# Kernel optimization log

Measured on AMD Instinct MI355X. Metric: run time of the kernel, lower is better.

Reference implementation:

```python
import jax, jax.numpy as jnp
import numpy as np

N = 100_000   # nodes
E = 1_600_000 # edges (avg degree 16)
D = 64        # node feature / conv width
L = 3         # num conv layers
M = 128       # final mlp hidden
BN_EPS = 1e-5


def setup_inputs() -> dict:
    key = jax.random.key(0)
    ks = jax.random.split(key, 12)
    s = np.float32(1.0 / np.sqrt(D))
    sm = np.float32(1.0 / np.sqrt(M))
    return dict(
        x=jax.random.normal(ks[0], (N, D), jnp.float32),
        edge_src=jax.random.randint(ks[1], (E,), 0, N, dtype=jnp.int32),
        edge_dst=jax.random.randint(ks[2], (E,), 0, N, dtype=jnp.int32),
        W1=jax.random.normal(ks[3], (L, D, D), jnp.float32) * s,
        b1=jnp.zeros((L, D), jnp.float32),
        g1=jnp.ones((L, D), jnp.float32),
        be1=jnp.zeros((L, D), jnp.float32),
        W2=jax.random.normal(ks[4], (L, D, D), jnp.float32) * s,
        b2=jnp.zeros((L, D), jnp.float32),
        eps_gin=jnp.zeros((L,), jnp.float32),  # train_eps=True, init 0
        g_bn=jnp.ones((L, D), jnp.float32),
        b_bn=jnp.zeros((L, D), jnp.float32),
        Wf1=jax.random.normal(ks[5], (D, M), jnp.float32) * s,
        bf1=jnp.zeros((M,), jnp.float32),
        gf=jnp.ones((M,), jnp.float32),
        bef=jnp.zeros((M,), jnp.float32),
        Wf2=jax.random.normal(ks[6], (M, 1), jnp.float32) * sm,
        bf2=jnp.zeros((1,), jnp.float32),
    )


def _bn(h, g, b):
    # BatchNorm1d training-mode forward over node dim (biased variance)
    m = h.mean(axis=0)
    v = h.var(axis=0)
    return (h - m) * jax.lax.rsqrt(v + BN_EPS) * g + b


def reference(x, edge_src, edge_dst, W1, b1, g1, be1, W2, b2, eps_gin,
              g_bn, b_bn, Wf1, bf1, gf, bef, Wf2, bf2):
    for i in range(L):
        # GIN aggregation: sum of neighbor features (scatter-add over edges)
        agg = jax.ops.segment_sum(x[edge_src], edge_dst, num_segments=N)
        h = (1.0 + eps_gin[i]) * x + agg
        # GIN nn: Linear -> BatchNorm -> LeakyReLU -> Linear
        h = h @ W1[i] + b1[i]
        h = jax.nn.leaky_relu(_bn(h, g1[i], be1[i]))  # slope 0.01 = torch default
        x = h @ W2[i] + b2[i]
        # outer BatchNorm + activation on all but last conv layer
        if i != L - 1:
            x = jax.nn.leaky_relu(_bn(x, g_bn[i], b_bn[i]))
    # final head: Linear -> BN -> LeakyReLU -> Linear(->1), flatten
    h = x @ Wf1 + bf1
    h = jax.nn.leaky_relu(_bn(h, gf, bef))
    out = h @ Wf2 + bf2
    return out.ravel()  # [N]
```

## Files before the change

### kernel.cpp

```cpp
#include <hip/hip_runtime.h>

#define LRELU(x) ((x) > 0.0f ? (x) : 0.01f * (x))
#define UAF __uint_as_float
#define NSLOT 16

#if defined(__has_builtin)
#if __has_builtin(__builtin_amdgcn_fdot2_f32_bf16)
#define HAS_DOT2BF 1
#endif
#endif
#ifndef HAS_DOT2BF
#define HAS_DOT2BF 0
#endif

__device__ inline uint pack_bf16_rne(float x, float y) {
    uint lo = __float_as_uint(x);
    uint hi = __float_as_uint(y);
    lo = (lo + 0x7fffu + ((lo >> 16) & 1u)) >> 16;
    hi = (hi + 0x7fffu + ((hi >> 16) & 1u)) & 0xffff0000u;
    return lo | hi;
}

__device__ inline float dot2bf(uint a, uint b, float c) {
#if HAS_DOT2BF
    typedef __bf16 bf16x2 __attribute__((ext_vector_type(2)));
    return __builtin_amdgcn_fdot2_f32_bf16(__builtin_bit_cast(bf16x2, a),
                                           __builtin_bit_cast(bf16x2, b), c, false);
#else
    c += UAF(a << 16) * UAF(b << 16);
    c += UAF(a & 0xffff0000u) * UAF(b & 0xffff0000u);
    return c;
#endif
}

__global__ void zero_kernel(float* p, int n) {
    int i = blockIdx.x * blockDim.x + threadIdx.x;
    if (i < n) p[i] = 0.0f;
}

__global__ __launch_bounds__(256) void bhist_kernel(const int* __restrict__ dst,
                                                    int* __restrict__ bcnt, int E, int NB) {
    __shared__ int h[512];
    for (int i = threadIdx.x; i < NB; i += 256) h[i] = 0;
    __syncthreads();
    int base = blockIdx.x * 8192;
    int end = min(E, base + 8192);
    for (int e = base + threadIdx.x; e < end; e += 256) atomicAdd(&h[dst[e] >> 8], 1);
    __syncthreads();
    for (int i = threadIdx.x; i < NB; i += 256)
        if (h[i]) atomicAdd(&bcnt[i], h[i]);
}

__global__ __launch_bounds__(512) void bscan_kernel(const int* __restrict__ bcnt,
                                                    int* __restrict__ boff,
                                                    int* __restrict__ bcur, int NB) {
    __shared__ int sh[512];
    int t = threadIdx.x;
    int v = (t < NB) ? bcnt[t] : 0;
    sh[t] = v;
    __syncthreads();
    for (int o = 1; o < 512; o <<= 1) {
        int u = (t >= o) ? sh[t - o] : 0;
        __syncthreads();
        sh[t] += u;
        __syncthreads();
    }
    if (t < NB) {
        boff[t] = sh[t] - v;
        bcur[t] = sh[t] - v;
    }
}

__global__ __launch_bounds__(256) void bscatter_kernel(const int* __restrict__ src,
                                                       const int* __restrict__ dst,
                                                       int* __restrict__ bcur,
                                                       uint* __restrict__ pairs, int E, int NB) {
    __shared__ int h[512];
    __shared__ int bbase[512];
    for (int i = threadIdx.x; i < NB; i += 256) h[i] = 0;
    __syncthreads();
    int base = blockIdx.x * 8192;
    int end = min(E, base + 8192);
    for (int e = base + threadIdx.x; e < end; e += 256) atomicAdd(&h[dst[e] >> 8], 1);
    __syncthreads();
    for (int i = threadIdx.x; i < NB; i += 256) {
        bbase[i] = h[i] ? atomicAdd(&bcur[i], h[i]) : 0;
        h[i] = 0;
    }
    __syncthreads();
    for (int e = base + threadIdx.x; e < end; e += 256) {
        int d = dst[e];
        int b = d >> 8;
        int o = atomicAdd(&h[b], 1);
        pairs[bbase[b] + o] = ((uint)src[e] << 8) | (uint)(d & 255);
    }
}

__global__ __launch_bounds__(256) void bcsr_kernel(const uint* __restrict__ pairs,
                                                   const int* __restrict__ boff,
                                                   int* __restrict__ ptr, int* __restrict__ cnt,
                                                   int* __restrict__ nbr, int N, int NB, int E) {
    __shared__ int h[256];
    __shared__ int sc[256];
    int b = blockIdx.x;
    int lo = boff[b];
    int hi = (b + 1 < NB) ? boff[b + 1] : E;
    int t = threadIdx.x;
    h[t] = 0;
    __syncthreads();
    for (int i = lo + t; i < hi; i += 256) atomicAdd(&h[pairs[i] & 255u], 1);
    __syncthreads();
    int v = h[t];
    sc[t] = v;
    __syncthreads();
    for (int o = 1; o < 256; o <<= 1) {
        int u = (t >= o) ? sc[t - o] : 0;
        __syncthreads();
        sc[t] += u;
        __syncthreads();
    }
    int excl = sc[t] - v;
    int node = (b << 8) + t;
    if (node < N) {
        ptr[node] = lo + excl;
        cnt[node] = v;
    }
    __syncthreads();
    h[t] = excl;
    __syncthreads();
    for (int i = lo + t; i < hi; i += 256) {
        uint p = pairs[i];
        int ld = p & 255u;
        int o = atomicAdd(&h[ld], 1);
        nbr[lo + o] = (int)(p >> 8);
    }
}

__global__ __launch_bounds__(256) void to_bf16_kernel(const float* __restrict__ in,
                                                      uint* __restrict__ table, int n8) {
    int i = blockIdx.x * blockDim.x + threadIdx.x;
    if (i >= n8) return;
    float4 a = *(const float4*)&in[(size_t)i * 8];
    float4 b = *(const float4*)&in[(size_t)i * 8 + 4];
    uint4 p = make_uint4(pack_bf16_rne(a.x, a.y), pack_bf16_rne(a.z, a.w),
                         pack_bf16_rne(b.x, b.y), pack_bf16_rne(b.z, b.w));
    *(uint4*)&table[(size_t)i * 4] = p;
}

__global__ void finalize_kernel(const float* __restrict__ sums, const float* __restrict__ g,
                                const float* __restrict__ be, float* __restrict__ scale,
                                float* __restrict__ shift, int C, float invN) {
    int d = threadIdx.x;
    if (d >= C) return;
    float s = 0.0f, s2 = 0.0f;
    for (int k = 0; k < NSLOT; k++) {
        s += sums[k * 2 * C + d];
        s2 += sums[k * 2 * C + C + d];
    }
    float mean = s * invN;
    float var = s2 * invN - mean * mean;
    float sc = g[d] * rsqrtf(var + 1e-5f);
    scale[d] = sc;
    shift[d] = be[d] - mean * sc;
}

template <bool ACT>
__global__ __launch_bounds__(256) void gather_kernel(
    const uint* __restrict__ tb, const int* __restrict__ ptr, const int* __restrict__ cnt,
    const int* __restrict__ nbr, const float* __restrict__ eps_gin, int layer,
    const float* __restrict__ scale, const float* __restrict__ shift, uint* __restrict__ agg,
    int N) {
    int gtid = blockIdx.x * blockDim.x + threadIdx.x;
    int node = gtid >> 6;
    if (node >= N) return;
    int lane = threadIdx.x & 63;
    int half = lane >> 5;
    int sl = lane & 31;
    float sc0 = 1.0f, sh0 = 0.0f, sc1 = 1.0f, sh1 = 0.0f;
    if (ACT) {
        sc0 = scale[2 * sl + 0];
        sh0 = shift[2 * sl + 0];
        sc1 = scale[2 * sl + 1];
        sh1 = shift[2 * sl + 1];
    }
    int start = ptr[node];
    int deg = cnt[node];
    float a0 = 0.0f, a1 = 0.0f;
    int j = half;
    for (; j + 14 < deg; j += 16) {
        int ni[8];
        uint vv[8];
#pragma unroll
        for (int q = 0; q < 8; q++) ni[q] = nbr[start + j + 2 * q];
#pragma unroll
        for (int q = 0; q < 8; q++) vv[q] = tb[(size_t)ni[q] * 32 + sl];
#pragma unroll
        for (int q = 0; q < 8; q++) {
            float f0 = UAF(vv[q] << 16), f1 = UAF(vv[q] & 0xffff0000u);
            if (ACT) {
                f0 = LRELU(f0 * sc0 + sh0);
                f1 = LRELU(f1 * sc1 + sh1);
            }
            a0 += f0;
            a1 += f1;
        }
    }
    for (; j + 6 < deg; j += 8) {
        int ni[4];
        uint vv[4];
#pragma unroll
        for (int q = 0; q < 4; q++) ni[q] = nbr[start + j + 2 * q];
#pragma unroll
        for (int q = 0; q < 4; q++) vv[q] = tb[(size_t)ni[q] * 32 + sl];
#pragma unroll
        for (int q = 0; q < 4; q++) {
            float f0 = UAF(vv[q] << 16), f1 = UAF(vv[q] & 0xffff0000u);
            if (ACT) {
                f0 = LRELU(f0 * sc0 + sh0);
                f1 = LRELU(f1 * sc1 + sh1);
            }
            a0 += f0;
            a1 += f1;
        }
    }
    for (; j < deg; j += 2) {
        uint vA = tb[(size_t)nbr[start + j] * 32 + sl];
        float f0 = UAF(vA << 16), f1 = UAF(vA & 0xffff0000u);
        if (ACT) {
            f0 = LRELU(f0 * sc0 + sh0);
            f1 = LRELU(f1 * sc1 + sh1);
        }
        a0 += f0;
        a1 += f1;
    }
    a0 += __shfl(a0, lane ^ 32);
    a1 += __shfl(a1, lane ^ 32);
    uint vs = tb[(size_t)node * 32 + sl];
    float s0 = UAF(vs << 16), s1 = UAF(vs & 0xffff0000u);
    if (ACT) {
        s0 = LRELU(s0 * sc0 + sh0);
        s1 = LRELU(s1 * sc1 + sh1);
    }
    float ep = 1.0f + eps_gin[layer];
    a0 += ep * s0;
    a1 += ep * s1;
    if (half == 0) agg[(size_t)node * 32 + sl] = pack_bf16_rne(a0, a1);
}

template <bool INBN, bool OUTB, int MINW>
__global__ __launch_bounds__(256, MINW) void gemm_bf16_kernel(
    const uint* __restrict__ inb, const float* __restrict__ inf, const float* __restrict__ W,
    const float* __restrict__ bias, const float* __restrict__ scale,
    const float* __restrict__ shift, uint* __restrict__ outb, float* __restrict__ outf,
    float* __restrict__ sums, int nrows) {
    constexpr int COLS = 64;
    __shared__ uint smem[32 * 68 + 32 * COLS];
    uint* inT = smem;
    uint* wsb = smem + 32 * 68;
    int t = threadIdx.x;
    int row0 = blockIdx.x * 64;

    if (!INBN) {
        for (int i = 0; i < 2; i++) {
            int f = t + 256 * i;
            int r = f >> 3, q = f & 7;
            int gr = row0 + r;
            uint4 v = make_uint4(0, 0, 0, 0);
            if (gr < nrows) v = *(const uint4*)&inb[(size_t)gr * 32 + q * 4];
            inT[(4 * q + 0) * 68 + r] = v.x;
            inT[(4 * q + 1) * 68 + r] = v.y;
            inT[(4 * q + 2) * 68 + r] = v.z;
            inT[(4 * q + 3) * 68 + r] = v.w;
        }
    } else {
        for (int i = 0; i < 4; i++) {
            int f = t + 256 * i;
            int r = f >> 4, q = f & 15;
            int gr = row0 + r;
            float4 v = make_float4(0.f, 0.f, 0.f, 0.f);
            if (gr < nrows) v = *(const float4*)&inf[(size_t)gr * 64 + q * 4];
            int d = 4 * q;
            float e0 = LRELU(v.x * scale[d + 0] + shift[d + 0]);
            float e1 = LRELU(v.y * scale[d + 1] + shift[d + 1]);
            float e2 = LRELU(v.z * scale[d + 2] + shift[d + 2]);
            float e3 = LRELU(v.w * scale[d + 3] + shift[d + 3]);
            inT[(2 * q + 0) * 68 + r] = pack_bf16_rne(e0, e1);
            inT[(2 * q + 1) * 68 + r] = pack_bf16_rne(e2, e3);
        }
    }
    for (int i = 0; i < COLS / 8; i++) {
        int f = t + 256 * i;
        int kp = f / COLS, c = f % COLS;
        wsb[kp * COLS + c] =
            pack_bf16_rne(W[(size_t)(2 * kp) * COLS + c], W[(size_t)(2 * kp + 1) * COLS + c]);
    }
    __syncthreads();

    int rg = t >> 4, cg = t & 15;
    int r0 = rg * 4, c0 = cg * 4;
    float acc[4][4];
#pragma unroll
    for (int r = 0; r < 4; r++)
#pragma unroll
        for (int c = 0; c < 4; c++) acc[r][c] = 0.0f;

#pragma unroll 8
    for (int kp = 0; kp < 32; kp++) {
        uint4 a = *(const uint4*)&inT[kp * 68 + r0];
        uint av[4] = {a.x, a.y, a.z, a.w};
        uint4 w = *(const uint4*)&wsb[kp * COLS + c0];
        uint wv[4] = {w.x, w.y, w.z, w.w};
#pragma unroll
        for (int r = 0; r < 4; r++)
#pragma unroll
            for (int c = 0; c < 4; c++) acc[r][c] = dot2bf(av[r], wv[c], acc[r][c]);
    }

    float ps[4], ps2[4];
#pragma unroll
    for (int c = 0; c < 4; c++) ps[c] = ps2[c] = 0.0f;
    float4 bv = *(const float4*)&bias[c0];
#pragma unroll
    for (int r = 0; r < 4; r++) {
        int gr = row0 + r0 + r;
        if (gr < nrows) {
            float o0 = acc[r][0] + bv.x;
            float o1 = acc[r][1] + bv.y;
            float o2 = acc[r][2] + bv.z;
            float o3 = acc[r][3] + bv.w;
            if (OUTB) {
                uint2 pk = make_uint2(pack_bf16_rne(o0, o1), pack_bf16_rne(o2, o3));
                *(uint2*)&outb[(size_t)gr * 32 + (c0 >> 1)] = pk;
            } else {
                *(float4*)&outf[(size_t)gr * 64 + c0] = make_float4(o0, o1, o2, o3);
            }
            ps[0] += o0;
            ps2[0] += o0 * o0;
            ps[1] += o1;
            ps2[1] += o1 * o1;
            ps[2] += o2;
            ps2[2] += o2 * o2;
            ps[3] += o3;
            ps2[3] += o3 * o3;
        }
    }

    if (sums == nullptr) return;

    __syncthreads();
    float* red = (float*)smem;
    float* red2 = red + 16 * COLS;
    *(float4*)&red[rg * COLS + c0] = *(float4*)&ps[0];
    *(float4*)&red2[rg * COLS + c0] = *(float4*)&ps2[0];
    __syncthreads();
    if (t < COLS) {
        float s = 0.0f, s2 = 0.0f;
#pragma unroll
        for (int j = 0; j < 16; j++) {
            s += red[j * COLS + t];
            s2 += red2[j * COLS + t];
        }
        int slot = blockIdx.x & (NSLOT - 1);
        atomicAdd(&sums[slot * 2 * COLS + t], s);
        atomicAdd(&sums[slot * 2 * COLS + COLS + t], s2);
    }
}

__global__ __launch_bounds__(256, 4) void gemm_f32_head_kernel(const float* __restrict__ in,
                                                               const float* __restrict__ W,
                                                               const float* __restrict__ bias,
                                                               float* __restrict__ out,
                                                               float* __restrict__ sums,
                                                               int nrows) {
    constexpr int COLS = 128;
    __shared__ float inT[64][68];
    __shared__ float ws[64][COLS];
    int t = threadIdx.x;
    int row0 = blockIdx.x * 64;

    for (int i = 0; i < 4; i++) {
        int f = t + 256 * i;
        int r = f >> 4, ch = f & 15;
        int gr = row0 + r;
        float4 v = make_float4(0.f, 0.f, 0.f, 0.f);
        if (gr < nrows) v = *(const float4*)&in[(size_t)gr * 64 + ch * 4];
        inT[ch * 4 + 0][r] = v.x;
        inT[ch * 4 + 1][r] = v.y;
        inT[ch * 4 + 2][r] = v.z;
        inT[ch * 4 + 3][r] = v.w;
    }
    for (int i = 0; i < COLS / 16; i++) {
        int f = t + 256 * i;
        int k = f / (COLS / 4), c4 = f % (COLS / 4);
        *(float4*)&ws[k][c4 * 4] = *(const float4*)&W[(size_t)k * COLS + c4 * 4];
    }
    __syncthreads();

    int rg = t >> 4, cg = t & 15;
    int r0 = rg * 4, c0 = cg * 4;
    float acc[4][8];
#pragma unroll
    for (int r = 0; r < 4; r++)
#pragma unroll
        for (int c = 0; c < 8; c++) acc[r][c] = 0.0f;

#pragma unroll 16
    for (int k = 0; k < 64; k++) {
        float4 a = *(const float4*)&inT[k][r0];
        float ar[4] = {a.x, a.y, a.z, a.w};
#pragma unroll
        for (int jj = 0; jj < 2; jj++) {
            float4 w4 = *(const float4*)&ws[k][c0 + jj * 64];
            float wr[4] = {w4.x, w4.y, w4.z, w4.w};
#pragma unroll
            for (int r = 0; r < 4; r++)
#pragma unroll
                for (int c = 0; c < 4; c++) acc[r][jj * 4 + c] += ar[r] * wr[c];
        }
    }

    float ps[8], ps2[8];
#pragma unroll
    for (int c = 0; c < 8; c++) ps[c] = ps2[c] = 0.0f;
#pragma unroll
    for (int r = 0; r < 4; r++) {
        int gr = row0 + r0 + r;
        if (gr < nrows) {
#pragma unroll
            for (int jj = 0; jj < 2; jj++) {
                float4 bv = *(const float4*)&bias[c0 + jj * 64];
                float4 o = make_float4(acc[r][jj * 4 + 0] + bv.x, acc[r][jj * 4 + 1] + bv.y,
                                       acc[r][jj * 4 + 2] + bv.z, acc[r][jj * 4 + 3] + bv.w);
                *(float4*)&out[(size_t)gr * COLS + c0 + jj * 64] = o;
                ps[jj * 4 + 0] += o.x;
                ps2[jj * 4 + 0] += o.x * o.x;
                ps[jj * 4 + 1] += o.y;
                ps2[jj * 4 + 1] += o.y * o.y;
                ps[jj * 4 + 2] += o.z;
                ps2[jj * 4 + 2] += o.z * o.z;
                ps[jj * 4 + 3] += o.w;
                ps2[jj * 4 + 3] += o.w * o.w;
            }
        }
    }

    __syncthreads();
    float* red = &inT[0][0];
    float* red2 = red + 16 * COLS;
#pragma unroll
    for (int jj = 0; jj < 2; jj++) {
        *(float4*)&red[rg * COLS + c0 + jj * 64] = *(float4*)&ps[jj * 4];
        *(float4*)&red2[rg * COLS + c0 + jj * 64] = *(float4*)&ps2[jj * 4];
    }
    __syncthreads();
    if (t < COLS) {
        float s = 0.0f, s2 = 0.0f;
#pragma unroll
        for (int j = 0; j < 16; j++) {
            s += red[j * COLS + t];
            s2 += red2[j * COLS + t];
        }
        int slot = blockIdx.x & (NSLOT - 1);
        atomicAdd(&sums[slot * 2 * COLS + t], s);
        atomicAdd(&sums[slot * 2 * COLS + COLS + t], s2);
    }
}

__global__ void head_out_kernel(const float* __restrict__ hf, const float* __restrict__ scale,
                                const float* __restrict__ shift, const float* __restrict__ Wf2,
                                const float* __restrict__ bf2, float* __restrict__ out,
                                int nrows) {
    int gtid = blockIdx.x * blockDim.x + threadIdx.x;
    int wid = gtid >> 6;
    int l = threadIdx.x & 63;
    if (wid >= nrows) return;
    float v0 = hf[(size_t)wid * 128 + l];
    float v1 = hf[(size_t)wid * 128 + 64 + l];
    v0 = LRELU(v0 * scale[l] + shift[l]);
    v1 = LRELU(v1 * scale[64 + l] + shift[64 + l]);
    float p = v0 * Wf2[l] + v1 * Wf2[64 + l];
    for (int o = 32; o > 0; o >>= 1) p += __shfl_down(p, o);
    if (l == 0) out[wid] = p + bf2[0];
}

extern "C" void kernel_launch(void* const* d_in, const int* in_sizes, int n_in, void* d_out,
                              int out_size, void* d_ws, size_t ws_size, hipStream_t stream) {
    const float* x = (const float*)d_in[0];
    const int* esrc = (const int*)d_in[1];
    const int* edst = (const int*)d_in[2];
    const float* W1 = (const float*)d_in[3];
    const float* b1 = (const float*)d_in[4];
    const float* g1 = (const float*)d_in[5];
    const float* be1 = (const float*)d_in[6];
    const float* W2 = (const float*)d_in[7];
    const float* b2 = (const float*)d_in[8];
    const float* eps_gin = (const float*)d_in[9];
    const float* g_bn = (const float*)d_in[10];
    const float* b_bn = (const float*)d_in[11];
    const float* Wf1 = (const float*)d_in[12];
    const float* bf1 = (const float*)d_in[13];
    const float* gf = (const float*)d_in[14];
    const float* bef = (const float*)d_in[15];
    const float* Wf2 = (const float*)d_in[16];
    const float* bf2 = (const float*)d_in[17];
    float* out = (float*)d_out;

    int N = in_sizes[0] / 64;
    int E = in_sizes[1];
    int NB = (N + 255) / 256;
    float invN = 1.0f / (float)N;

    float* ws = (float*)d_ws;
    size_t ND = (size_t)N * 64;
    uint* table = (uint*)ws;
    uint* pairs = (uint*)(ws + ND / 2);
    float* X = ws;
    float* h1 = ws + ND;
    uint* agg = (uint*)(ws + 2 * ND);
    float* HF = ws + ND;
    float* stats = ws + 3 * ND;
    float* ssarea = stats + 5 * NSLOT * 128 + NSLOT * 256;
    int* ibase = (int*)(ssarea + 5 * 128 + 256);
    int* bcnt = ibase;
    int* bcur = ibase + 512;
    int* boff = ibase + 1024;
    int* cnt = ibase + 1536;
    int* ptr = cnt + N;
    int* nbr = ptr + N;

    int nzero = 5 * NSLOT * 128 + NSLOT * 256 + 5 * 128 + 256 + 512;
    zero_kernel<<<(nzero + 255) / 256, 256, 0, stream>>>(stats, nzero);

    int eb = (E + 8191) / 8192;
    bhist_kernel<<<eb, 256, 0, stream>>>(edst, bcnt, E, NB);
    bscan_kernel<<<1, 512, 0, stream>>>(bcnt, boff, bcur, NB);
    bscatter_kernel<<<eb, 256, 0, stream>>>(esrc, edst, bcur, pairs, E, NB);
    bcsr_kernel<<<NB, 256, 0, stream>>>(pairs, boff, ptr, cnt, nbr, N, NB, E);

    int n8 = N * 8;
    int gg = (N + 63) / 64;
    int gblocks = (N * 64 + 255) / 256;
    to_bf16_kernel<<<(n8 + 255) / 256, 256, 0, stream>>>(x, table, n8);

    for (int i = 0; i < 3; i++) {
        float* st = stats + (size_t)(2 * i) * NSLOT * 128;
        float* so = stats + (size_t)(2 * i + 1) * NSLOT * 128;
        float* st_ss = ssarea + (size_t)(2 * i) * 128;
        float* so_ss = ssarea + (size_t)(2 * i + 1) * 128;
        if (i == 0) {
            gather_kernel<false><<<gblocks, 256, 0, stream>>>(table, ptr, cnt, nbr, eps_gin, i,
                                                              nullptr, nullptr, agg, N);
        } else {
            float* sp_ss = ssarea + (size_t)(2 * (i - 1) + 1) * 128;
            gather_kernel<true><<<gblocks, 256, 0, stream>>>(table, ptr, cnt, nbr, eps_gin, i,
                                                             sp_ss, sp_ss + 64, agg, N);
        }
        gemm_bf16_kernel<false, false, 6><<<gg, 256, 0, stream>>>(
            agg, nullptr, W1 + (size_t)i * 4096, b1 + (size_t)i * 64, nullptr, nullptr, nullptr,
            h1, st, N);
        finalize_kernel<<<1, 64, 0, stream>>>(st, g1 + (size_t)i * 64, be1 + (size_t)i * 64,
                                              st_ss, st_ss + 64, 64, invN);
        if (i < 2) {
            gemm_bf16_kernel<true, true, 6><<<gg, 256, 0, stream>>>(
                nullptr, h1, W2 + (size_t)i * 4096, b2 + (size_t)i * 64, st_ss, st_ss + 64,
                table, nullptr, so, N);
            finalize_kernel<<<1, 64, 0, stream>>>(so, g_bn + (size_t)i * 64,
                                                  b_bn + (size_t)i * 64, so_ss, so_ss + 64, 64,
                                                  invN);
        } else {
            gemm_bf16_kernel<true, false, 6><<<gg, 256, 0, stream>>>(
                nullptr, h1, W2 + (size_t)i * 4096, b2 + (size_t)i * 64, st_ss, st_ss + 64,
                nullptr, X, nullptr, N);
        }
    }

    float* sf = stats + (size_t)5 * NSLOT * 128;
    float* sf_ss = ssarea + 5 * 128;
    gemm_f32_head_kernel<<<gg, 256, 0, stream>>>(X, Wf1, bf1, HF, sf, N);
    finalize_kernel<<<1, 128, 0, stream>>>(sf, gf, bef, sf_ss, sf_ss + 128, 128, invN);
    head_out_kernel<<<(N + 3) / 4, 256, 0, stream>>>(HF, sf_ss, sf_ss + 128, Wf2, bf2, out, N);
}
```

Measured before the change: 382.2 us.

## Split bf16 node table into feature-quarter planes and prepack GEMM weights

```diff
diff --git a/kernel.cpp b/kernel.cpp
--- a/kernel.cpp
+++ b/kernel.cpp
@@ -136,15 +136,101 @@
     }
 }
 
+__global__ void packw_kernel(const float* __restrict__ W1, const float* __restrict__ W2,
+                             uint* __restrict__ Wp) {
+    int id = blockIdx.x * blockDim.x + threadIdx.x;
+    if (id >= 6 * 2048) return;
+    int mat = id >> 11;
+    int r = id & 2047;
+    int kp = r >> 6, c = r & 63;
+    const float* Ws = (mat < 3) ? (W1 + (size_t)mat * 4096) : (W2 + (size_t)(mat - 3) * 4096);
+    Wp[id] = pack_bf16_rne(Ws[(size_t)(2 * kp) * 64 + c], Ws[(size_t)(2 * kp + 1) * 64 + c]);
+}
+
 __global__ __launch_bounds__(256) void to_bf16_kernel(const float* __restrict__ in,
-                                                      uint* __restrict__ table, int n8) {
+                                                      uint* __restrict__ planes, int n8,
+                                                      int NQ) {
     int i = blockIdx.x * blockDim.x + threadIdx.x;
     if (i >= n8) return;
     float4 a = *(const float4*)&in[(size_t)i * 8];
     float4 b = *(const float4*)&in[(size_t)i * 8 + 4];
     uint4 p = make_uint4(pack_bf16_rne(a.x, a.y), pack_bf16_rne(a.z, a.w),
                          pack_bf16_rne(b.x, b.y), pack_bf16_rne(b.z, b.w));
-    *(uint4*)&table[(size_t)i * 4] = p;
+    int node = i >> 3;
+    int oct = i & 7;
+    int q = oct >> 1;
+    int off = (oct & 1) * 4;
+    *(uint4*)&planes[(size_t)q * NQ + (size_t)node * 8 + off] = p;
+}
+
+template <bool ACT>
+__global__ __launch_bounds__(256) void gather_kernel(
+    const uint* __restrict__ planes, const int* __restrict__ ptr, const int* __restrict__ cnt,
+    const int* __restrict__ nbr, const float* __restrict__ eps_gin, int layer,
+    const float* __restrict__ scale, const float* __restrict__ shift, uint* __restrict__ agg,
+    int N, int NQ) {
+    int q = blockIdx.x & 3;
+    int node = (blockIdx.x >> 2) * 4 + (threadIdx.x >> 6);
+    if (node >= N) return;
+    const uint* tb = planes + (size_t)q * NQ;
+    int lane = threadIdx.x & 63;
+    int sub = lane >> 3;
+    int fl = lane & 7;
+    float sc0 = 1.0f, sh0 = 0.0f, sc1 = 1.0f, sh1 = 0.0f;
+    if (ACT) {
+        int p = 2 * (q * 8 + fl);
+        sc0 = scale[p + 0];
+        sh0 = shift[p + 0];
+        sc1 = scale[p + 1];
+        sh1 = shift[p + 1];
+    }
+    int start = ptr[node];
+    int deg = cnt[node];
+    float a0 = 0.0f, a1 = 0.0f;
+    int j = sub;
+    for (; j + 8 < deg; j += 16) {
+        int nA = nbr[start + j];
+        int nB = nbr[start + j + 8];
+        uint vA = tb[(size_t)nA * 8 + fl];
+        uint vB = tb[(size_t)nB * 8 + fl];
+        float fA0 = UAF(vA << 16), fA1 = UAF(vA & 0xffff0000u);
+        float fB0 = UAF(vB << 16), fB1 = UAF(vB & 0xffff0000u);
+        if (ACT) {
+            fA0 = LRELU(fA0 * sc0 + sh0);
+            fA1 = LRELU(fA1 * sc1 + sh1);
+            fB0 = LRELU(fB0 * sc0 + sh0);
+            fB1 = LRELU(fB1 * sc1 + sh1);
+        }
+        a0 += fA0 + fB0;
+        a1 += fA1 + fB1;
+    }
+    for (; j < deg; j += 8) {
+        int nA = nbr[start + j];
+        uint vA = tb[(size_t)nA * 8 + fl];
+        float fA0 = UAF(vA << 16), fA1 = UAF(vA & 0xffff0000u);
+        if (ACT) {
+            fA0 = LRELU(fA0 * sc0 + sh0);
+            fA1 = LRELU(fA1 * sc1 + sh1);
+        }
+        a0 += fA0;
+        a1 += fA1;
+    }
+    for (int o = 8; o < 64; o <<= 1) {
+        a0 += __shfl_xor(a0, o);
+        a1 += __shfl_xor(a1, o);
+    }
+    if (sub == 0) {
+        uint vs = tb[(size_t)node * 8 + fl];
+        float s0 = UAF(vs << 16), s1 = UAF(vs & 0xffff0000u);
+        if (ACT) {
+            s0 = LRELU(s0 * sc0 + sh0);
+            s1 = LRELU(s1 * sc1 + sh1);
+        }
+        float ep = 1.0f + eps_gin[layer];
+        a0 += ep * s0;
+        a1 += ep * s1;
+        agg[(size_t)node * 32 + q * 8 + fl] = pack_bf16_rne(a0, a1);
+    }
 }
 
 __global__ void finalize_kernel(const float* __restrict__ sums, const float* __restrict__ g,
@@ -164,95 +250,12 @@
     shift[d] = be[d] - mean * sc;
 }
 
-template <bool ACT>
-__global__ __launch_bounds__(256) void gather_kernel(
-    const uint* __restrict__ tb, const int* __restrict__ ptr, const int* __restrict__ cnt,
-    const int* __restrict__ nbr, const float* __restrict__ eps_gin, int layer,
-    const float* __restrict__ scale, const float* __restrict__ shift, uint* __restrict__ agg,
-    int N) {
-    int gtid = blockIdx.x * blockDim.x + threadIdx.x;
-    int node = gtid >> 6;
-    if (node >= N) return;
-    int lane = threadIdx.x & 63;
-    int half = lane >> 5;
-    int sl = lane & 31;
-    float sc0 = 1.0f, sh0 = 0.0f, sc1 = 1.0f, sh1 = 0.0f;
-    if (ACT) {
-        sc0 = scale[2 * sl + 0];
-        sh0 = shift[2 * sl + 0];
-        sc1 = scale[2 * sl + 1];
-        sh1 = shift[2 * sl + 1];
-    }
-    int start = ptr[node];
-    int deg = cnt[node];
-    float a0 = 0.0f, a1 = 0.0f;
-    int j = half;
-    for (; j + 14 < deg; j += 16) {
-        int ni[8];
-        uint vv[8];
-#pragma unroll
-        for (int q = 0; q < 8; q++) ni[q] = nbr[start + j + 2 * q];
-#pragma unroll
-        for (int q = 0; q < 8; q++) vv[q] = tb[(size_t)ni[q] * 32 + sl];
-#pragma unroll
-        for (int q = 0; q < 8; q++) {
-            float f0 = UAF(vv[q] << 16), f1 = UAF(vv[q] & 0xffff0000u);
-            if (ACT) {
-                f0 = LRELU(f0 * sc0 + sh0);
-                f1 = LRELU(f1 * sc1 + sh1);
-            }
-            a0 += f0;
-            a1 += f1;
-        }
-    }
-    for (; j + 6 < deg; j += 8) {
-        int ni[4];
-        uint vv[4];
-#pragma unroll
-        for (int q = 0; q < 4; q++) ni[q] = nbr[start + j + 2 * q];
-#pragma unroll
-        for (int q = 0; q < 4; q++) vv[q] = tb[(size_t)ni[q] * 32 + sl];
-#pragma unroll
-        for (int q = 0; q < 4; q++) {
-            float f0 = UAF(vv[q] << 16), f1 = UAF(vv[q] & 0xffff0000u);
-            if (ACT) {
-                f0 = LRELU(f0 * sc0 + sh0);
-                f1 = LRELU(f1 * sc1 + sh1);
-            }
-            a0 += f0;
-            a1 += f1;
-        }
-    }
-    for (; j < deg; j += 2) {
-        uint vA = tb[(size_t)nbr[start + j] * 32 + sl];
-        float f0 = UAF(vA << 16), f1 = UAF(vA & 0xffff0000u);
-        if (ACT) {
-            f0 = LRELU(f0 * sc0 + sh0);
-            f1 = LRELU(f1 * sc1 + sh1);
-        }
-        a0 += f0;
-        a1 += f1;
-    }
-    a0 += __shfl(a0, lane ^ 32);
-    a1 += __shfl(a1, lane ^ 32);
-    uint vs = tb[(size_t)node * 32 + sl];
-    float s0 = UAF(vs << 16), s1 = UAF(vs & 0xffff0000u);
-    if (ACT) {
-        s0 = LRELU(s0 * sc0 + sh0);
-        s1 = LRELU(s1 * sc1 + sh1);
-    }
-    float ep = 1.0f + eps_gin[layer];
-    a0 += ep * s0;
-    a1 += ep * s1;
-    if (half == 0) agg[(size_t)node * 32 + sl] = pack_bf16_rne(a0, a1);
-}
-
 template <bool INBN, bool OUTB, int MINW>
 __global__ __launch_bounds__(256, MINW) void gemm_bf16_kernel(
-    const uint* __restrict__ inb, const float* __restrict__ inf, const float* __restrict__ W,
+    const uint* __restrict__ inb, const float* __restrict__ inf, const uint* __restrict__ Wp,
     const float* __restrict__ bias, const float* __restrict__ scale,
     const float* __restrict__ shift, uint* __restrict__ outb, float* __restrict__ outf,
-    float* __restrict__ sums, int nrows) {
+    float* __restrict__ sums, int nrows, int NQ) {
     constexpr int COLS = 64;
     __shared__ uint smem[32 * 68 + 32 * COLS];
     uint* inT = smem;
@@ -288,11 +291,9 @@
             inT[(2 * q + 1) * 68 + r] = pack_bf16_rne(e2, e3);
         }
     }
-    for (int i = 0; i < COLS / 8; i++) {
-        int f = t + 256 * i;
-        int kp = f / COLS, c = f % COLS;
-        wsb[kp * COLS + c] =
-            pack_bf16_rne(W[(size_t)(2 * kp) * COLS + c], W[(size_t)(2 * kp + 1) * COLS + c]);
+    for (int i = 0; i < 2; i++) {
+        int f = (t + 256 * i) * 4;
+        *(uint4*)&wsb[f] = *(const uint4*)&Wp[f];
     }
     __syncthreads();
 
@@ -330,7 +331,7 @@
             float o3 = acc[r][3] + bv.w;
             if (OUTB) {
                 uint2 pk = make_uint2(pack_bf16_rne(o0, o1), pack_bf16_rne(o2, o3));
-                *(uint2*)&outb[(size_t)gr * 32 + (c0 >> 1)] = pk;
+                *(uint2*)&outb[(size_t)(c0 >> 4) * NQ + (size_t)gr * 8 + ((c0 & 15) >> 1)] = pk;
             } else {
                 *(float4*)&outf[(size_t)gr * 64 + c0] = make_float4(o0, o1, o2, o3);
             }
@@ -508,11 +509,12 @@
     int N = in_sizes[0] / 64;
     int E = in_sizes[1];
     int NB = (N + 255) / 256;
+    int NQ = N * 8;
     float invN = 1.0f / (float)N;
 
     float* ws = (float*)d_ws;
     size_t ND = (size_t)N * 64;
-    uint* table = (uint*)ws;
+    uint* planes = (uint*)ws;
     uint* pairs = (uint*)(ws + ND / 2);
     float* X = ws;
     float* h1 = ws + ND;
@@ -527,6 +529,7 @@
     int* cnt = ibase + 1536;
     int* ptr = cnt + N;
     int* nbr = ptr + N;
+    uint* Wp = (uint*)(nbr + E);
 
     int nzero = 5 * NSLOT * 128 + NSLOT * 256 + 5 * 128 + 256 + 512;
     zero_kernel<<<(nzero + 255) / 256, 256, 0, stream>>>(stats, nzero);
@@ -536,11 +539,12 @@
     bscan_kernel<<<1, 512, 0, stream>>>(bcnt, boff, bcur, NB);
     bscatter_kernel<<<eb, 256, 0, stream>>>(esrc, edst, bcur, pairs, E, NB);
     bcsr_kernel<<<NB, 256, 0, stream>>>(pairs, boff, ptr, cnt, nbr, N, NB, E);
+    packw_kernel<<<(6 * 2048 + 255) / 256, 256, 0, stream>>>(W1, W2, Wp);
 
     int n8 = N * 8;
     int gg = (N + 63) / 64;
-    int gblocks = (N * 64 + 255) / 256;
-    to_bf16_kernel<<<(n8 + 255) / 256, 256, 0, stream>>>(x, table, n8);
+    int gblocks = ((N + 3) / 4) * 4;
+    to_bf16_kernel<<<(n8 + 255) / 256, 256, 0, stream>>>(x, planes, n8, NQ);
 
     for (int i = 0; i < 3; i++) {
         float* st = stats + (size_t)(2 * i) * NSLOT * 128;
@@ -548,29 +552,29 @@
         float* st_ss = ssarea + (size_t)(2 * i) * 128;
         float* so_ss = ssarea + (size_t)(2 * i + 1) * 128;
         if (i == 0) {
-            gather_kernel<false><<<gblocks, 256, 0, stream>>>(table, ptr, cnt, nbr, eps_gin, i,
-                                                              nullptr, nullptr, agg, N);
+            gather_kernel<false><<<gblocks, 256, 0, stream>>>(
+                planes, ptr, cnt, nbr, eps_gin, i, nullptr, nullptr, agg, N, NQ);
         } else {
             float* sp_ss = ssarea + (size_t)(2 * (i - 1) + 1) * 128;
-            gather_kernel<true><<<gblocks, 256, 0, stream>>>(table, ptr, cnt, nbr, eps_gin, i,
-                                                             sp_ss, sp_ss + 64, agg, N);
+            gather_kernel<true><<<gblocks, 256, 0, stream>>>(
+                planes, ptr, cnt, nbr, eps_gin, i, sp_ss, sp_ss + 64, agg, N, NQ);
         }
         gemm_bf16_kernel<false, false, 6><<<gg, 256, 0, stream>>>(
-            agg, nullptr, W1 + (size_t)i * 4096, b1 + (size_t)i * 64, nullptr, nullptr, nullptr,
-            h1, st, N);
+            agg, nullptr, Wp + (size_t)i * 2048, b1 + (size_t)i * 64, nullptr, nullptr, nullptr,
+            h1, st, N, NQ);
         finalize_kernel<<<1, 64, 0, stream>>>(st, g1 + (size_t)i * 64, be1 + (size_t)i * 64,
                                               st_ss, st_ss + 64, 64, invN);
         if (i < 2) {
             gemm_bf16_kernel<true, true, 6><<<gg, 256, 0, stream>>>(
-                nullptr, h1, W2 + (size_t)i * 4096, b2 + (size_t)i * 64, st_ss, st_ss + 64,
-                table, nullptr, so, N);
+                nullptr, h1, Wp + (size_t)(3 + i) * 2048, b2 + (size_t)i * 64, st_ss, st_ss + 64,
+                planes, nullptr, so, N, NQ);
             finalize_kernel<<<1, 64, 0, stream>>>(so, g_bn + (size_t)i * 64,
                                                   b_bn + (size_t)i * 64, so_ss, so_ss + 64, 64,
                                                   invN);
         } else {
             gemm_bf16_kernel<true, false, 6><<<gg, 256, 0, stream>>>(
-                nullptr, h1, W2 + (size_t)i * 4096, b2 + (size_t)i * 64, st_ss, st_ss + 64,
-                nullptr, X, nullptr, N);
+                nullptr, h1, Wp + (size_t)(3 + i) * 2048, b2 + (size_t)i * 64, st_ss, st_ss + 64,
+                nullptr, X, nullptr, N, NQ);
         }
     }
 
```

Result: slower. 579.9 us (+51.7%).
